# Performance work log

Measured on AMD Instinct MI355X. Metric: run time of the kernel, lower is better.

The kernel has to match this reference:

```python
import jax, jax.numpy as jnp
import numpy as np

B, S, M = 4, 4096, 2048
LATENT, H, D = 512, 16, 128  # latent_dim, num_heads, hidden_dim (per-head)


def setup_inputs() -> dict:
    key = jax.random.key(0)
    ks = jax.random.split(key, 12)
    sd = lambda fan_in: 1.0 / np.sqrt(fan_in)
    return {
        "x": jax.random.normal(ks[0], (B, S, M), dtype=jnp.float32),
        # k path: down-proj to latent, up-proj to H*D (vmapped Dense pair, slice 0)
        "Wd_k": jax.random.normal(ks[1], (M, LATENT), dtype=jnp.float32) * sd(M),
        "bd_k": jnp.zeros((LATENT,), dtype=jnp.float32),
        "Wu_k": jax.random.normal(ks[2], (LATENT, H * D), dtype=jnp.float32) * sd(LATENT),
        "bu_k": jnp.zeros((H * D,), dtype=jnp.float32),
        # v path (slice 1 of the vmapped params)
        "Wd_v": jax.random.normal(ks[3], (M, LATENT), dtype=jnp.float32) * sd(M),
        "bd_v": jnp.zeros((LATENT,), dtype=jnp.float32),
        "Wu_v": jax.random.normal(ks[4], (LATENT, H * D), dtype=jnp.float32) * sd(LATENT),
        "bu_v": jnp.zeros((H * D,), dtype=jnp.float32),
        # q projection
        "Wq": jax.random.normal(ks[5], (M, H * D), dtype=jnp.float32) * sd(M),
        "bq": jnp.zeros((H * D,), dtype=jnp.float32),
        # output projection
        "Wo": jax.random.normal(ks[6], (H * D, M), dtype=jnp.float32) * sd(H * D),
        "bo": jnp.zeros((M,), dtype=jnp.float32),
    }


def reference(x, Wd_k, bd_k, Wu_k, bu_k, Wd_v, bd_v, Wu_v, bu_v, Wq, bq, Wo, bo):
    b, s, m = x.shape
    # low-rank KV: down-project to latent cache, up-project to heads
    cache_k = x @ Wd_k + bd_k                      # [B,S,L]
    cache_v = x @ Wd_v + bd_v                      # [B,S,L]
    k = (cache_k @ Wu_k + bu_k).reshape(b, s, H, D)
    v = (cache_v @ Wu_v + bu_v).reshape(b, s, H, D)
    q = (x @ Wq + bq).reshape(b, s, H, D)
    # NOTE: source permutes k as (0,1,3,2) on [B,S,H,D] -> scores are per-token
    # head-vs-head [B,S,H,H], softmax over the last (head) axis.
    sim = jnp.einsum("bshd,bsgd->bshg", q, k) * (D ** -0.5)
    attn = jax.nn.softmax(sim, axis=-1)            # [B,S,H,H]
    out = jnp.einsum("bshg,bsgd->bshd", attn, v)   # [B,S,H,D]
    out = out.reshape(b, s, H * D)
    return out @ Wo + bo                           # [B,S,M]
```

## Files before the change

kernel.cpp:

```cpp
#include <hip/hip_runtime.h>

typedef __attribute__((ext_vector_type(8))) short short8v;
typedef __attribute__((ext_vector_type(4))) float f32x4;
typedef __attribute__((ext_vector_type(4))) unsigned int uint4v;

#define GLOBAL_AS(p) ((const __attribute__((address_space(1))) void*)(p))
#define LDS_AS(p)    ((__attribute__((address_space(3))) void*)(p))
#define WAITV(n) asm volatile("s_waitcnt vmcnt(" #n ")" ::: "memory")
#define BARRIER() __builtin_amdgcn_s_barrier()

__device__ __forceinline__ unsigned short f2bf(float f) {
  unsigned int u = __builtin_bit_cast(unsigned int, f);
  u += 0x7fffu + ((u >> 16) & 1u);
  return (unsigned short)(u >> 16);
}
__device__ __forceinline__ float bf2f(unsigned short u) {
  unsigned int x = ((unsigned int)u) << 16;
  return __builtin_bit_cast(float, x);
}

__global__ __launch_bounds__(256) void transpose_all(
    const float* __restrict__ Wq, const float* __restrict__ Wo,
    const float* __restrict__ Wd_k, const float* __restrict__ Wd_v,
    const float* __restrict__ Wu_k, const float* __restrict__ Wu_v,
    unsigned short* __restrict__ w1t, unsigned short* __restrict__ w2t,
    unsigned short* __restrict__ w3t) {
  int b = blockIdx.x;
  const float* src; unsigned short* dst; int K, N, ntx;
  if (b < 4096)      { src = Wq;   dst = w1t + 1024 * 2048; K = 2048; N = 2048; ntx = 64; }
  else if (b < 8192) { src = Wo;   dst = w3t;               K = 2048; N = 2048; ntx = 64; b -= 4096; }
  else if (b < 9216) { src = Wd_k; dst = w1t;               K = 2048; N = 512;  ntx = 16; b -= 8192; }
  else if (b < 10240){ src = Wd_v; dst = w1t + 512 * 2048;  K = 2048; N = 512;  ntx = 16; b -= 9216; }
  else if (b < 11264){ src = Wu_k; dst = w2t;               K = 512;  N = 2048; ntx = 64; b -= 10240; }
  else               { src = Wu_v; dst = w2t + 2048 * 512;  K = 512;  N = 2048; ntx = 64; b -= 11264; }
  __shared__ float tile[32][33];
  const int bx = b % ntx, by = b / ntx;
  const int tx = threadIdx.x & 31, ty = threadIdx.x >> 5;
  const int k0 = by * 32, n0 = bx * 32;
#pragma unroll
  for (int i = 0; i < 32; i += 8)
    tile[ty + i][tx] = src[(size_t)(k0 + ty + i) * N + n0 + tx];
  __syncthreads();
#pragma unroll
  for (int i = 0; i < 32; i += 8)
    dst[(size_t)(n0 + ty + i) * K + k0 + tx] = f2bf(tile[tx][ty + i]);
}

__global__ __launch_bounds__(256) void cvt_f32_bf16(
    const float* __restrict__ s, unsigned short* __restrict__ d) {
  const int o = blockIdx.x;
  const size_t row = (size_t)((o & 7) * 2048 + (o >> 3));
  size_t i = row * 2048 + threadIdx.x * 8;
  f32x4 v0 = *(const f32x4*)(s + i);
  f32x4 v1 = *(const f32x4*)(s + i + 4);
  union U8 { uint4v v; unsigned short us[8]; } o8;
  o8.us[0] = f2bf(v0.x); o8.us[1] = f2bf(v0.y); o8.us[2] = f2bf(v0.z); o8.us[3] = f2bf(v0.w);
  o8.us[4] = f2bf(v1.x); o8.us[5] = f2bf(v1.y); o8.us[6] = f2bf(v1.z); o8.us[7] = f2bf(v1.w);
  *(uint4v*)(d + i) = o8.v;
}

__global__ __launch_bounds__(256) void fill_bias(
    const float* __restrict__ bd_k, const float* __restrict__ bd_v,
    const float* __restrict__ bq, const float* __restrict__ bu_k,
    const float* __restrict__ bu_v, float* __restrict__ b1, float* __restrict__ b2) {
  int i = blockIdx.x * 256 + threadIdx.x;
  if (i < 512) b1[i] = bd_k[i];
  else if (i < 1024) b1[i] = bd_v[i - 512];
  else if (i < 3072) b1[i] = bq[i - 1024];
  else if (i < 5120) b2[i - 3072] = bu_k[i - 3072];
  else if (i < 7168) b2[i - 3072] = bu_v[i - 5120];
}

template <int OUT_BF16>
__global__ __launch_bounds__(256, 2) void gemm_bt(
    const unsigned short* __restrict__ A, int lda, int nsplit_col, int acol_off,
    const unsigned short* __restrict__ Bt, int ldb,
    const float* __restrict__ bias, void* __restrict__ Cp, int ldc,
    int K, int ntn) {
  __shared__ unsigned short Als[2][256 * 64];
  __shared__ unsigned short Bls[128 * 64];
  const int t = threadIdx.x;
  const int lane = t & 63, wave = t >> 6;

  const int qx = gridDim.x >> 3;
  const int bid = (blockIdx.x & 7) * qx + (blockIdx.x >> 3);
  const int bm = (bid / ntn) * 256;
  const int bn = (bid % ntn) * 128;
  const unsigned short* Ab = A + (bn >= nsplit_col ? acol_off : 0);

  const int wr = wave >> 1, wc = wave & 1;
  const int g = lane >> 4, r = lane & 15;
  const int swz = r & 7;
  const int NT = K >> 6;

  f32x4 acc[8][4];
#pragma unroll
  for (int i = 0; i < 8; ++i)
#pragma unroll
    for (int j = 0; j < 4; ++j) acc[i][j] = (f32x4){0.f, 0.f, 0.f, 0.f};

  const int srow = t >> 3;
  const int jsrc = (t & 7) ^ (srow & 7);
  const unsigned short* aptr = Ab + (size_t)(bm + srow) * lda + (jsrc << 3);
  const unsigned short* bptr = Bt + (size_t)(bn + srow) * ldb + (jsrc << 3);
  const int wbase = wave * 512;

  auto stageA = [&](int kt, int buf) {
    const unsigned short* ak = aptr + (size_t)kt * 64;
#pragma unroll
    for (int u = 0; u < 8; ++u)
      __builtin_amdgcn_global_load_lds(GLOBAL_AS(ak + (size_t)(u * 32) * lda),
                                       LDS_AS(&Als[buf][u * 2048 + wbase]), 16, 0, 0);
  };
  auto stageB = [&](int kt) {
    const unsigned short* bk = bptr + (size_t)kt * 64;
#pragma unroll
    for (int u = 0; u < 4; ++u)
      __builtin_amdgcn_global_load_lds(GLOBAL_AS(bk + (size_t)(u * 32) * ldb),
                                       LDS_AS(&Bls[u * 2048 + wbase]), 16, 0, 0);
  };

  stageA(0, 0);
  stageB(0);
  if (NT > 1) stageA(1, 1);

  for (int T = 0; T < NT; ++T) {
    if (T + 1 < NT) { WAITV(8); } else { WAITV(0); }
    BARRIER();
    const unsigned short* la = Als[T & 1];
#pragma unroll
    for (int ks = 0; ks < 2; ++ks) {
      const int c16 = (((ks << 2) + g) ^ swz) << 3;
      short8v bf[4];
#pragma unroll
      for (int ni = 0; ni < 4; ++ni)
        bf[ni] = *(const short8v*)&Bls[(wc * 64 + ni * 16 + r) * 64 + c16];
      __builtin_amdgcn_s_setprio(1);
#pragma unroll
      for (int mi = 0; mi < 8; ++mi) {
        short8v af = *(const short8v*)&la[(wr * 128 + mi * 16 + r) * 64 + c16];
#pragma unroll
        for (int ni = 0; ni < 4; ++ni)
          acc[mi][ni] = __builtin_amdgcn_mfma_f32_16x16x32_bf16(
              af, bf[ni], acc[mi][ni], 0, 0, 0);
      }
      __builtin_amdgcn_s_setprio(0);
    }
    BARRIER();
    if (T + 1 < NT) {
      stageB(T + 1);
      if (T + 2 < NT) stageA(T + 2, T & 1);
    }
  }

#pragma unroll
  for (int ni = 0; ni < 4; ++ni) {
    const int col = bn + wc * 64 + ni * 16 + r;
    const float bv = bias[col];
#pragma unroll
    for (int mi = 0; mi < 8; ++mi) {
      const int row0 = bm + wr * 128 + mi * 16 + (g << 2);
#pragma unroll
      for (int j = 0; j < 4; ++j) {
        float v = acc[mi][ni][j] + bv;
        if (OUT_BF16)
          ((unsigned short*)Cp)[(size_t)(row0 + j) * ldc + col] = f2bf(v);
        else
          ((float*)Cp)[(size_t)(row0 + j) * ldc + col] = v;
      }
    }
  }
}

__global__ __launch_bounds__(256) void attn_kernel(
    const unsigned short* __restrict__ out1, const unsigned short* __restrict__ kv,
    unsigned short* __restrict__ aout) {
  const int o = blockIdx.x;
  const int s = (o & 7) * 2048 + (o >> 3);
  const int t = threadIdx.x;
  __shared__ float qs[16 * 132], ks2[16 * 132], vs[16 * 132];
  __shared__ float attn[256];
  const int h = t >> 4, d0 = (t & 15) * 8;

  union U8 { uint4v v; unsigned short us[8]; };
  U8 qv, kv8, vv;
  qv.v = *(const uint4v*)(out1 + (size_t)s * 3072 + 1024 + t * 8);
  kv8.v = *(const uint4v*)(kv + (size_t)s * 4096 + t * 8);
  vv.v = *(const uint4v*)(kv + (size_t)s * 4096 + 2048 + t * 8);
#pragma unroll
  for (int j = 0; j < 8; ++j) {
    qs[h * 132 + d0 + j] = bf2f(qv.us[j]);
    ks2[h * 132 + d0 + j] = bf2f(kv8.us[j]);
    vs[h * 132 + d0 + j] = bf2f(vv.us[j]);
  }
  __syncthreads();

  const int gg0 = t & 15;
  const f32x4* qrow = (const f32x4*)&qs[h * 132];
  const f32x4* krow = (const f32x4*)&ks2[gg0 * 132];
  float acc = 0.f;
#pragma unroll
  for (int dd = 0; dd < 32; ++dd) {
    f32x4 a4 = qrow[dd], b4 = krow[dd];
    acc += a4.x * b4.x + a4.y * b4.y + a4.z * b4.z + a4.w * b4.w;
  }
  acc *= 0.08838834764831845f;
  float mx = acc;
#pragma unroll
  for (int ofs = 8; ofs; ofs >>= 1) mx = fmaxf(mx, __shfl_xor(mx, ofs));
  float e = __expf(acc - mx);
  float sm = e;
#pragma unroll
  for (int ofs = 8; ofs; ofs >>= 1) sm += __shfl_xor(sm, ofs);
  attn[t] = e / sm;
  __syncthreads();

  f32x4 o0 = (f32x4){0.f, 0.f, 0.f, 0.f}, o1 = (f32x4){0.f, 0.f, 0.f, 0.f};
#pragma unroll
  for (int gg = 0; gg < 16; ++gg) {
    const float a = attn[(h << 4) + gg];
    f32x4 v0 = *(const f32x4*)&vs[gg * 132 + d0];
    f32x4 v1 = *(const f32x4*)&vs[gg * 132 + d0 + 4];
    o0 += v0 * a;
    o1 += v1 * a;
  }
  U8 ov;
  ov.us[0] = f2bf(o0.x); ov.us[1] = f2bf(o0.y); ov.us[2] = f2bf(o0.z); ov.us[3] = f2bf(o0.w);
  ov.us[4] = f2bf(o1.x); ov.us[5] = f2bf(o1.y); ov.us[6] = f2bf(o1.z); ov.us[7] = f2bf(o1.w);
  *(uint4v*)(aout + (size_t)s * 2048 + t * 8) = ov.v;
}

extern "C" void kernel_launch(void* const* d_in, const int* in_sizes, int n_in,
                              void* d_out, int out_size, void* d_ws, size_t ws_size,
                              hipStream_t stream) {
  (void)in_sizes; (void)n_in; (void)out_size; (void)ws_size;
  const float* x    = (const float*)d_in[0];
  const float* Wd_k = (const float*)d_in[1];
  const float* bd_k = (const float*)d_in[2];
  const float* Wu_k = (const float*)d_in[3];
  const float* bu_k = (const float*)d_in[4];
  const float* Wd_v = (const float*)d_in[5];
  const float* bd_v = (const float*)d_in[6];
  const float* Wu_v = (const float*)d_in[7];
  const float* bu_v = (const float*)d_in[8];
  const float* Wq   = (const float*)d_in[9];
  const float* bq   = (const float*)d_in[10];
  const float* Wo   = (const float*)d_in[11];
  const float* bo   = (const float*)d_in[12];

  char* ws = (char*)d_ws;
  unsigned short* w1t  = (unsigned short*)(ws);
  unsigned short* w2t  = (unsigned short*)(ws + 12582912);
  unsigned short* w3t  = (unsigned short*)(ws + 16777216);
  float*          b1   = (float*)(ws + 25165824);
  float*          b2   = (float*)(ws + 25178112);
  unsigned short* xb   = (unsigned short*)(ws + 25194496);
  unsigned short* out1 = (unsigned short*)(ws + 92303360);
  unsigned short* kvb  = (unsigned short*)(ws + 192966656);
  unsigned short* attO = xb;

  dim3 blk(256);

  transpose_all<<<dim3(12288), blk, 0, stream>>>(Wq, Wo, Wd_k, Wd_v, Wu_k, Wu_v,
                                                 w1t, w2t, w3t);
  fill_bias<<<dim3(28), blk, 0, stream>>>(bd_k, bd_v, bq, bu_k, bu_v, b1, b2);

  cvt_f32_bf16<<<dim3(16384), blk, 0, stream>>>(x, xb);

  gemm_bt<1><<<dim3(64 * 24), blk, 0, stream>>>(
      xb, 2048, 1 << 30, 0, w1t, 2048, b1, out1, 3072, 2048, 24);

  gemm_bt<1><<<dim3(64 * 32), blk, 0, stream>>>(
      out1, 3072, 2048, 512, w2t, 512, b2, kvb, 4096, 512, 32);

  attn_kernel<<<dim3(16384), blk, 0, stream>>>(out1, kvb, attO);

  gemm_bt<0><<<dim3(64 * 16), blk, 0, stream>>>(
      attO, 2048, 1 << 30, 0, w3t, 2048, bo, (float*)d_out, 2048, 2048, 16);
}
```

Baseline: 571.7 us.

## Rewrite GEMM as 256x256 tile with 8 waves and interleaved load/MFMA schedule

The bf16 GEMM moves from a 256x128 tile with 4 waves to a 256x256 tile with 8 waves (512 threads), with A and B both double-buffered in LDS. The K loop is unrolled by two and split into quarter-phases: each phase reads an A sub-block from LDS, issues part of the next tile's global-to-LDS loads, then runs its MFMAs between barriers and sched_barriers. The goal is better operand reuse per tile and overlap of memory traffic with matrix math. In exchange it uses 128KB of LDS per block, limiting occupancy to one block per CU, and adds many barriers per K step. Grids are halved to match the wider N tile.

```diff
diff --git a/kernel.cpp b/kernel.cpp
--- a/kernel.cpp
+++ b/kernel.cpp
@@ -7,7 +7,9 @@
 #define GLOBAL_AS(p) ((const __attribute__((address_space(1))) void*)(p))
 #define LDS_AS(p)    ((__attribute__((address_space(3))) void*)(p))
 #define WAITV(n) asm volatile("s_waitcnt vmcnt(" #n ")" ::: "memory")
+#define LGKM0()  asm volatile("s_waitcnt lgkmcnt(0)" ::: "memory")
 #define BARRIER() __builtin_amdgcn_s_barrier()
+#define SCHED0() __builtin_amdgcn_sched_barrier(0)
 
 __device__ __forceinline__ unsigned short f2bf(float f) {
   unsigned int u = __builtin_bit_cast(unsigned int, f);
@@ -72,25 +74,25 @@
 }
 
 template <int OUT_BF16>
-__global__ __launch_bounds__(256, 2) void gemm_bt(
+__global__ __launch_bounds__(512, 2) void gemm_bt(
     const unsigned short* __restrict__ A, int lda, int nsplit_col, int acol_off,
     const unsigned short* __restrict__ Bt, int ldb,
     const float* __restrict__ bias, void* __restrict__ Cp, int ldc,
     int K, int ntn) {
-  __shared__ unsigned short Als[2][256 * 64];
-  __shared__ unsigned short Bls[128 * 64];
+  __shared__ unsigned short lds[2][2][256 * 64];
   const int t = threadIdx.x;
   const int lane = t & 63, wave = t >> 6;
 
   const int qx = gridDim.x >> 3;
   const int bid = (blockIdx.x & 7) * qx + (blockIdx.x >> 3);
   const int bm = (bid / ntn) * 256;
-  const int bn = (bid % ntn) * 128;
+  const int bn = (bid % ntn) * 256;
   const unsigned short* Ab = A + (bn >= nsplit_col ? acol_off : 0);
 
-  const int wr = wave >> 1, wc = wave & 1;
+  const int wr = wave >> 2, wc = wave & 3;
   const int g = lane >> 4, r = lane & 15;
-  const int swz = r & 7;
+  const int c16_0 = (g ^ (r & 7)) << 3;
+  const int c16_1 = ((4 + g) ^ (r & 7)) << 3;
   const int NT = K >> 6;
 
   f32x4 acc[8][4];
@@ -99,58 +101,117 @@
 #pragma unroll
     for (int j = 0; j < 4; ++j) acc[i][j] = (f32x4){0.f, 0.f, 0.f, 0.f};
 
-  const int srow = t >> 3;
-  const int jsrc = (t & 7) ^ (srow & 7);
-  const unsigned short* aptr = Ab + (size_t)(bm + srow) * lda + (jsrc << 3);
-  const unsigned short* bptr = Bt + (size_t)(bn + srow) * ldb + (jsrc << 3);
+  const int trow = t >> 3;
+  const int jsrc = (t & 7) ^ (trow & 7);
+  const unsigned short* aptr = Ab + (size_t)(bm + trow) * lda + (jsrc << 3);
+  const unsigned short* bptr = Bt + (size_t)(bn + trow) * ldb + (jsrc << 3);
   const int wbase = wave * 512;
 
-  auto stageA = [&](int kt, int buf) {
-    const unsigned short* ak = aptr + (size_t)kt * 64;
-#pragma unroll
-    for (int u = 0; u < 8; ++u)
-      __builtin_amdgcn_global_load_lds(GLOBAL_AS(ak + (size_t)(u * 32) * lda),
-                                       LDS_AS(&Als[buf][u * 2048 + wbase]), 16, 0, 0);
-  };
-  auto stageB = [&](int kt) {
-    const unsigned short* bk = bptr + (size_t)kt * 64;
-#pragma unroll
-    for (int u = 0; u < 4; ++u)
-      __builtin_amdgcn_global_load_lds(GLOBAL_AS(bk + (size_t)(u * 32) * ldb),
-                                       LDS_AS(&Bls[u * 2048 + wbase]), 16, 0, 0);
-  };
-
-  stageA(0, 0);
-  stageB(0);
-  if (NT > 1) stageA(1, 1);
-
-  for (int T = 0; T < NT; ++T) {
-    if (T + 1 < NT) { WAITV(8); } else { WAITV(0); }
-    BARRIER();
-    const unsigned short* la = Als[T & 1];
-#pragma unroll
-    for (int ks = 0; ks < 2; ++ks) {
-      const int c16 = (((ks << 2) + g) ^ swz) << 3;
-      short8v bf[4];
+  auto stageA = [&](int kt, int h2) {
+    unsigned short* dst = &lds[kt & 1][0][h2 * 8192 + wbase];
+    const unsigned short* src = aptr + (size_t)(h2 * 128) * lda + kt * 64;
+    __builtin_amdgcn_global_load_lds(GLOBAL_AS(src), LDS_AS(dst), 16, 0, 0);
+    __builtin_amdgcn_global_load_lds(GLOBAL_AS(src + (size_t)64 * lda),
+                                     LDS_AS(dst + 4096), 16, 0, 0);
+  };
+  auto stageB = [&](int kt, int h2) {
+    unsigned short* dst = &lds[kt & 1][1][h2 * 8192 + wbase];
+    const unsigned short* src = bptr + (size_t)(h2 * 128) * ldb + kt * 64;
+    __builtin_amdgcn_global_load_lds(GLOBAL_AS(src), LDS_AS(dst), 16, 0, 0);
+    __builtin_amdgcn_global_load_lds(GLOBAL_AS(src + (size_t)64 * ldb),
+                                     LDS_AS(dst + 4096), 16, 0, 0);
+  };
+
+  short8v bq[4][2], aq[2][2];
+  auto readB = [&](const unsigned short* lb) {
+#pragma unroll
+    for (int ni = 0; ni < 4; ++ni) {
+      bq[ni][0] = *(const short8v*)&lb[(wc * 64 + ni * 16 + r) * 64 + c16_0];
+      bq[ni][1] = *(const short8v*)&lb[(wc * 64 + ni * 16 + r) * 64 + c16_1];
+    }
+  };
+  auto readA = [&](const unsigned short* la, int q) {
+#pragma unroll
+    for (int mi = 0; mi < 2; ++mi) {
+      aq[mi][0] = *(const short8v*)&la[(wr * 128 + q * 32 + mi * 16 + r) * 64 + c16_0];
+      aq[mi][1] = *(const short8v*)&la[(wr * 128 + q * 32 + mi * 16 + r) * 64 + c16_1];
+    }
+  };
+  auto MF = [&](int q) {
+    __builtin_amdgcn_s_setprio(1);
+#pragma unroll
+    for (int mi = 0; mi < 2; ++mi)
 #pragma unroll
       for (int ni = 0; ni < 4; ++ni)
-        bf[ni] = *(const short8v*)&Bls[(wc * 64 + ni * 16 + r) * 64 + c16];
-      __builtin_amdgcn_s_setprio(1);
-#pragma unroll
-      for (int mi = 0; mi < 8; ++mi) {
-        short8v af = *(const short8v*)&la[(wr * 128 + mi * 16 + r) * 64 + c16];
-#pragma unroll
-        for (int ni = 0; ni < 4; ++ni)
-          acc[mi][ni] = __builtin_amdgcn_mfma_f32_16x16x32_bf16(
-              af, bf[ni], acc[mi][ni], 0, 0, 0);
-      }
-      __builtin_amdgcn_s_setprio(0);
-    }
-    BARRIER();
-    if (T + 1 < NT) {
-      stageB(T + 1);
-      if (T + 2 < NT) stageA(T + 2, T & 1);
-    }
+#pragma unroll
+        for (int ks = 0; ks < 2; ++ks)
+          acc[q * 2 + mi][ni] = __builtin_amdgcn_mfma_f32_16x16x32_bf16(
+              aq[mi][ks], bq[ni][ks], acc[q * 2 + mi][ni], 0, 0, 0);
+    __builtin_amdgcn_s_setprio(0);
+  };
+
+  stageA(0, 0); stageA(0, 1); stageB(0, 0); stageB(0, 1);
+  stageA(1, 0); stageA(1, 1); stageB(1, 0); stageB(1, 1);
+  WAITV(8);
+  BARRIER();
+
+  for (int t2 = 0; t2 < NT; t2 += 2) {
+    const bool sA1 = (t2 > 0);
+    const bool sN = (t2 + 2 < NT);
+    const unsigned short* la0 = lds[0][0];
+    const unsigned short* lb0 = lds[0][1];
+    const unsigned short* la1 = lds[1][0];
+    const unsigned short* lb1 = lds[1][1];
+
+    readB(lb0); readA(la0, 0);
+    if (sA1) stageA(t2 + 1, 0);
+    BARRIER(); LGKM0(); SCHED0();
+    MF(0);
+    BARRIER();
+
+    readA(la0, 1);
+    if (sA1) stageA(t2 + 1, 1);
+    BARRIER(); LGKM0(); SCHED0();
+    MF(1);
+    BARRIER();
+
+    readA(la0, 2);
+    if (sN) stageB(t2 + 2, 0);
+    BARRIER(); LGKM0(); SCHED0();
+    MF(2);
+    BARRIER();
+
+    readA(la0, 3);
+    if (sN) stageB(t2 + 2, 1);
+    BARRIER(); LGKM0(); SCHED0();
+    MF(3);
+    if (sN) { WAITV(4); } else { WAITV(0); }
+    BARRIER();
+
+    readB(lb1); readA(la1, 0);
+    if (sN) stageA(t2 + 2, 0);
+    BARRIER(); LGKM0(); SCHED0();
+    MF(0);
+    BARRIER();
+
+    readA(la1, 1);
+    if (sN) stageA(t2 + 2, 1);
+    BARRIER(); LGKM0(); SCHED0();
+    MF(1);
+    BARRIER();
+
+    readA(la1, 2);
+    if (sN) stageB(t2 + 3, 0);
+    BARRIER(); LGKM0(); SCHED0();
+    MF(2);
+    BARRIER();
+
+    readA(la1, 3);
+    if (sN) stageB(t2 + 3, 1);
+    BARRIER(); LGKM0(); SCHED0();
+    MF(3);
+    if (sN) { WAITV(4); } else { WAITV(0); }
+    BARRIER();
   }
 
 #pragma unroll
@@ -267,14 +328,14 @@
 
   cvt_f32_bf16<<<dim3(16384), blk, 0, stream>>>(x, xb);
 
-  gemm_bt<1><<<dim3(64 * 24), blk, 0, stream>>>(
-      xb, 2048, 1 << 30, 0, w1t, 2048, b1, out1, 3072, 2048, 24);
-
-  gemm_bt<1><<<dim3(64 * 32), blk, 0, stream>>>(
-      out1, 3072, 2048, 512, w2t, 512, b2, kvb, 4096, 512, 32);
+  gemm_bt<1><<<dim3(64 * 12), dim3(512), 0, stream>>>(
+      xb, 2048, 1 << 30, 0, w1t, 2048, b1, out1, 3072, 2048, 12);
+
+  gemm_bt<1><<<dim3(64 * 16), dim3(512), 0, stream>>>(
+      out1, 3072, 2048, 512, w2t, 512, b2, kvb, 4096, 512, 16);
 
   attn_kernel<<<dim3(16384), blk, 0, stream>>>(out1, kvb, attO);
 
-  gemm_bt<0><<<dim3(64 * 16), blk, 0, stream>>>(
-      attO, 2048, 1 << 30, 0, w3t, 2048, bo, (float*)d_out, 2048, 2048, 16);
-}
+  gemm_bt<0><<<dim3(64 * 8), dim3(512), 0, stream>>>(
+      attO, 2048, 1 << 30, 0, w3t, 2048, bo, (float*)d_out, 2048, 2048, 8);
+}
```

Result: no change. 578.1 us (median of 2 runs) (+1.1%).
